# Kernel optimization log

Measured on AMD Instinct MI355X. Metric: run time of the kernel, lower is better.

Reference implementation:

```python
import jax, jax.numpy as jnp
import numpy as np
import math

B, L, H, U = 4, 4096, 1024, 1024


def setup_inputs() -> dict:
    key = jax.random.key(0)
    k_in, k_wi, k_bi, k_wo, k_bo, k_u = jax.random.split(key, 6)
    inputs = jax.random.normal(k_in, (B, L, H), dtype=jnp.float32)
    # Linear layers (torch Linear: y = x @ W.T + b), scaled like torch default init
    Wi = jax.random.normal(k_wi, (U, H), dtype=jnp.float32) / math.sqrt(H)
    bi = jax.random.normal(k_bi, (U,), dtype=jnp.float32) * 0.01
    Wo = jax.random.normal(k_wo, (H, U), dtype=jnp.float32) / math.sqrt(U)
    bo = jax.random.normal(k_bo, (H,), dtype=jnp.float32) * 0.01
    # LRU-style init of nu_log / gamma_log, exactly as in the torch __init__
    r_min, r_max = 0.9, 0.999
    u = jax.random.uniform(k_u, (U,), dtype=jnp.float32)
    nu_log = jnp.log(-0.5 * jnp.log(u * (r_max ** 2 - r_min ** 2) + r_min ** 2))
    gamma_log = jnp.log(jnp.sqrt(1.0 - jnp.exp(-jnp.exp(nu_log)) ** 2))
    params_log = jnp.stack([nu_log, gamma_log])  # [2, U]
    return {"inputs": inputs, "Wi": Wi, "bi": bi, "Wo": Wo, "bo": bo,
            "params_log": params_log}


def reference(inputs, Wi, bi, Wo, bo, params_log):
    # u = i_dense(inputs): [B, L, U]
    u = jnp.einsum('blh,uh->blu', inputs, Wi) + bi
    params = jnp.exp(params_log)
    nu, gamma = params[0], params[1]  # each [U]

    log2_L = int(np.ceil(np.log2(L)))
    pad_len = 2 ** log2_L - L
    x = jnp.pad(u, ((0, 0), (0, pad_len), (0, 0))) if pad_len else u
    Lp = 2 ** log2_L

    # Log-depth doubling parallel scan: h_t = exp(-nu) * h_{t-1} + u_t
    for i in range(1, log2_L + 1):
        l = 2 ** i
        x = x.reshape(B * Lp // l, l, U)
        x1, x2 = x[:, : l // 2], x[:, l // 2:]
        pos = jnp.arange(1, l // 2 + 1, dtype=jnp.float32)  # [l/2]
        lambs = jnp.exp(-pos[:, None] * nu)                  # [l/2, U]
        x2 = x2 + lambs * x1[:, -1:]
        x = jnp.concatenate([x1, x2], axis=1).reshape(B, Lp, U)

    x = x[:, :L] * gamma
    # o_dense: [B, L, H]
    return jnp.einsum('blu,hu->blh', x, Wo) + bo
```

## Files before the change

kernel.cpp:

```cpp
#include <hip/hip_runtime.h>

#define B_DIM 4
#define L_DIM 4096
#define H_DIM 1024
#define U_DIM 1024
#define M_DIM (B_DIM * L_DIM)
#define LC 64
#define NCH (L_DIM / LC)

using f32x4  = __attribute__((ext_vector_type(4))) float;
using bf16x8 = __attribute__((ext_vector_type(8))) __bf16;
using us8    = __attribute__((ext_vector_type(8))) unsigned short;

__device__ inline unsigned short f32_to_bf16(float f) {
  unsigned int u = __float_as_uint(f);
  u += 0x7FFF + ((u >> 16) & 1);
  return (unsigned short)(u >> 16);
}
__device__ inline float bf16_to_f32(unsigned short v) {
  return __uint_as_float((unsigned int)v << 16);
}

__device__ inline void async_load16(const void* g, void* l) {
  __builtin_amdgcn_global_load_lds(
      (const __attribute__((address_space(1))) void*)g,
      (__attribute__((address_space(3))) void*)l, 16, 0, 0);
}

#define IN_ELEMS  (M_DIM * H_DIM)
#define WI_ELEMS  (U_DIM * H_DIM)
#define WO_ELEMS  (H_DIM * U_DIM)
#define CVT_TOTAL (IN_ELEMS + WI_ELEMS + WO_ELEMS)

__global__ __launch_bounds__(256) void cvt_all(
    const float* __restrict__ inp, const float* __restrict__ wi,
    const float* __restrict__ wo,
    unsigned short* __restrict__ inp_b, unsigned short* __restrict__ wi_b,
    unsigned short* __restrict__ wo_b)
{
  size_t e = ((size_t)blockIdx.x * 256 + threadIdx.x) * 8;
  if (e >= CVT_TOTAL) return;
  const float* src; unsigned short* dst; size_t off;
  if (e < IN_ELEMS)                 { src = inp; dst = inp_b; off = e; }
  else if (e < IN_ELEMS + WI_ELEMS) { src = wi;  dst = wi_b;  off = e - IN_ELEMS; }
  else                              { src = wo;  dst = wo_b;  off = e - IN_ELEMS - WI_ELEMS; }
  f32x4 a = *(const f32x4*)(src + off);
  f32x4 b = *(const f32x4*)(src + off + 4);
  us8 r;
  r[0] = f32_to_bf16(a.x); r[1] = f32_to_bf16(a.y);
  r[2] = f32_to_bf16(a.z); r[3] = f32_to_bf16(a.w);
  r[4] = f32_to_bf16(b.x); r[5] = f32_to_bf16(b.y);
  r[6] = f32_to_bf16(b.z); r[7] = f32_to_bf16(b.w);
  *(us8*)(dst + off) = r;
}

#define TM 128
#define TN 128
#define BK 32

template <typename OUT, bool CARRY, int K>
__global__ __launch_bounds__(256) void gemm_bt_bias(
    const unsigned short* __restrict__ A, const unsigned short* __restrict__ Bm,
    const float* __restrict__ bias, OUT* __restrict__ C,
    int M, int N,
    float* __restrict__ carry_out, const float* __restrict__ params_log)
{
  __shared__ __attribute__((aligned(16))) unsigned short sA[2][TM * BK];
  __shared__ __attribute__((aligned(16))) unsigned short sB[2][TN * BK];

  const int tid    = threadIdx.x;
  const int lane   = tid & 63;
  const int wave   = tid >> 6;
  const int wm     = wave & 1;
  const int wn     = wave >> 1;
  const int frag_m = lane & 15;
  const int quad   = lane >> 4;
  const int frag_kb = 16 * (quad ^ ((lane >> 1) & 3));

  const int p    = blockIdx.y * gridDim.x + blockIdx.x;
  const int xcd  = p & 7;
  const int j    = p >> 3;
  const int slab = gridDim.y >> 3;
  const int by   = xcd * slab + (j % slab);
  const int bx   = j / slab;

  const int m0 = by * TM;
  const int n0 = bx * TN;

  const char* Ab = (const char*)A;
  const char* Bb = (const char*)Bm;
  const size_t rowbytes = (size_t)K * 2;

  const int r0s  = tid >> 2;
  const int r1s  = r0s + 64;
  const int csw  = 16 * ((tid & 3) ^ ((tid >> 3) & 3));
  const int o0   = tid * 16;
  const int o1   = o0 + 4096;

  f32x4 acc[4][4];
  #pragma unroll
  for (int i = 0; i < 4; ++i)
    #pragma unroll
    for (int jj = 0; jj < 4; ++jj)
      acc[i][jj] = {0.f, 0.f, 0.f, 0.f};

  auto stage = [&](int s, int kk) {
    const size_t kb = (size_t)kk * 2;
    async_load16(Ab + (size_t)(m0 + r0s) * rowbytes + kb + csw, (char*)sA[s] + o0);
    async_load16(Ab + (size_t)(m0 + r1s) * rowbytes + kb + csw, (char*)sA[s] + o1);
    async_load16(Bb + (size_t)(n0 + r0s) * rowbytes + kb + csw, (char*)sB[s] + o0);
    async_load16(Bb + (size_t)(n0 + r1s) * rowbytes + kb + csw, (char*)sB[s] + o1);
  };

  constexpr int NI = K / BK;
  stage(0, 0);

  #pragma unroll 2
  for (int i = 0; i < NI; ++i) {
    if (i + 1 < NI) {
      stage((i + 1) & 1, (i + 1) * BK);
      asm volatile("s_waitcnt vmcnt(4)\n\ts_barrier" ::: "memory");
    } else {
      asm volatile("s_waitcnt vmcnt(0)\n\ts_barrier" ::: "memory");
    }

    const int s = i & 1;
    bf16x8 af[4], bf[4];
    #pragma unroll
    for (int mi = 0; mi < 4; ++mi)
      af[mi] = *(const bf16x8*)((const char*)sA[s] + (wm * 64 + mi * 16 + frag_m) * 64 + frag_kb);
    #pragma unroll
    for (int ni = 0; ni < 4; ++ni)
      bf[ni] = *(const bf16x8*)((const char*)sB[s] + (wn * 64 + ni * 16 + frag_m) * 64 + frag_kb);

    #pragma unroll
    for (int mi = 0; mi < 4; ++mi)
      #pragma unroll
      for (int ni = 0; ni < 4; ++ni)
        acc[mi][ni] = __builtin_amdgcn_mfma_f32_16x16x32_bf16(af[mi], bf[ni], acc[mi][ni], 0, 0, 0);

    asm volatile("s_barrier" ::: "memory");
  }

  const int rr0 = quad * 4;
  #pragma unroll
  for (int ni = 0; ni < 4; ++ni) {
    int col  = n0 + wn * 64 + ni * 16 + frag_m;
    float bv = bias[col];
    #pragma unroll
    for (int mi = 0; mi < 4; ++mi) {
      int rowb = m0 + wm * 64 + mi * 16 + rr0;
      #pragma unroll
      for (int r = 0; r < 4; ++r) {
        float v = acc[mi][ni][r] + bv;
        if constexpr (sizeof(OUT) == 2)
          C[(size_t)(rowb + r) * N + col] = (OUT)f32_to_bf16(v);
        else
          C[(size_t)(rowb + r) * N + col] = (OUT)v;
      }
    }
  }

  if constexpr (CARRY) {
    const int chunk = (m0 >> 6) + wm;
    #pragma unroll
    for (int ni = 0; ni < 4; ++ni) {
      int col  = n0 + wn * 64 + ni * 16 + frag_m;
      float bv = bias[col];
      float nu = expf(params_log[col]);
      float w_base = expf(-nu * (float)(63 - quad * 4));
      float linv   = expf(nu);
      float l16inv = expf(16.f * nu);
      float part = 0.f;
      float wmi  = w_base;
      #pragma unroll
      for (int mi = 0; mi < 4; ++mi) {
        float w = wmi;
        #pragma unroll
        for (int r = 0; r < 4; ++r) {
          part = fmaf(w, acc[mi][ni][r] + bv, part);
          w *= linv;
        }
        wmi *= l16inv;
      }
      part += __shfl_xor(part, 16);
      part += __shfl_xor(part, 32);
      if (quad == 0)
        carry_out[(size_t)chunk * U_DIM + col] = part;
    }
  }
}

__global__ __launch_bounds__(256) void scan_prefix(
    const float* __restrict__ carry, const float* __restrict__ params_log,
    float* __restrict__ prefix)
{
  int t  = blockIdx.x * 256 + threadIdx.x;
  int b  = t >> 10;
  int uu = t & (U_DIM - 1);
  float lp = expf(-expf(params_log[uu]) * (float)LC);
  const float* cp = carry  + (size_t)b * NCH * U_DIM + uu;
  float*       pp = prefix + (size_t)b * NCH * U_DIM + uu;
  float vals[NCH];
  #pragma unroll
  for (int c = 0; c < NCH; ++c)
    vals[c] = cp[(size_t)c * U_DIM];
  float s = 0.f;
  #pragma unroll
  for (int c = 0; c < NCH; ++c) {
    pp[(size_t)c * U_DIM] = s;
    s = fmaf(s, lp, vals[c]);
  }
}

__global__ __launch_bounds__(256) void scan_apply(
    const unsigned short* __restrict__ u, const float* __restrict__ params_log,
    const float* __restrict__ prefix, unsigned short* __restrict__ x_b)
{
  int uu = blockIdx.x * 256 + threadIdx.x;
  int c  = blockIdx.y;
  int b  = blockIdx.z;
  float l = expf(-expf(params_log[uu]));
  float g = expf(params_log[U_DIM + uu]);
  float s = prefix[((size_t)b * NCH + c) * U_DIM + uu];
  const unsigned short* p = u + (size_t)(b * L_DIM + c * LC) * U_DIM + uu;
  unsigned short* q = x_b + (size_t)(b * L_DIM + c * LC) * U_DIM + uu;
  #pragma unroll 8
  for (int j = 0; j < LC; ++j) {
    s = fmaf(s, l, bf16_to_f32(p[(size_t)j * U_DIM]));
    q[(size_t)j * U_DIM] = f32_to_bf16(s * g);
  }
}

extern "C" void kernel_launch(void* const* d_in, const int* in_sizes, int n_in,
                              void* d_out, int out_size, void* d_ws, size_t ws_size,
                              hipStream_t stream)
{
  const float* inputs     = (const float*)d_in[0];
  const float* Wi         = (const float*)d_in[1];
  const float* bi         = (const float*)d_in[2];
  const float* Wo         = (const float*)d_in[3];
  const float* bo         = (const float*)d_in[4];
  const float* params_log = (const float*)d_in[5];
  float* out = (float*)d_out;

  char* ws = (char*)d_ws;
  unsigned short* u_b    = (unsigned short*)(ws);
  unsigned short* x_b    = (unsigned short*)(ws + (32u << 20));
  unsigned short* in_b   = (unsigned short*)(ws + (64u << 20));
  unsigned short* wi_b   = (unsigned short*)(ws + (96u << 20));
  unsigned short* wo_b   = (unsigned short*)(ws + (98u << 20));
  float*          carry  = (float*)(ws + (100u << 20));
  float*          prefix = (float*)(ws + (101u << 20));

  cvt_all<<<dim3((CVT_TOTAL / 8 + 255) / 256), 256, 0, stream>>>(
      inputs, Wi, Wo, in_b, wi_b, wo_b);

  gemm_bt_bias<unsigned short, true, H_DIM>
      <<<dim3(U_DIM / TN, M_DIM / TM), 256, 0, stream>>>(
      in_b, wi_b, bi, u_b, M_DIM, U_DIM, carry, params_log);

  scan_prefix<<<dim3(B_DIM * U_DIM / 256),     256, 0, stream>>>(carry, params_log, prefix);
  scan_apply <<<dim3(U_DIM / 256, NCH, B_DIM), 256, 0, stream>>>(u_b, params_log, prefix, x_b);

  gemm_bt_bias<float, false, U_DIM>
      <<<dim3(H_DIM / TN, M_DIM / TM), 256, 0, stream>>>(
      x_b, wo_b, bo, out, M_DIM, H_DIM, nullptr, nullptr);
}
```

Measured before the change: 253.6 us.

## Replace async global-to-LDS loads with register-staged prefetch in GEMM

The GEMM main loop no longer uses global_load_lds direct-to-LDS copies. It now prefetches the next K-tile into registers, runs the MFMAs on the current LDS buffer, then writes the registers into the other LDS buffer and synchronizes. The goal is to overlap global loads with compute through register staging and to drop the explicit vmcnt waits. The cost is more VGPRs and extra LDS write instructions, which could lower occupancy.

```diff
diff --git a/kernel.cpp b/kernel.cpp
--- a/kernel.cpp
+++ b/kernel.cpp
@@ -19,12 +19,6 @@
 }
 __device__ inline float bf16_to_f32(unsigned short v) {
   return __uint_as_float((unsigned int)v << 16);
-}
-
-__device__ inline void async_load16(const void* g, void* l) {
-  __builtin_amdgcn_global_load_lds(
-      (const __attribute__((address_space(1))) void*)g,
-      (__attribute__((address_space(3))) void*)l, 16, 0, 0);
 }
 
 #define IN_ELEMS  (M_DIM * H_DIM)
@@ -91,11 +85,11 @@
   const char* Bb = (const char*)Bm;
   const size_t rowbytes = (size_t)K * 2;
 
-  const int r0s  = tid >> 2;
-  const int r1s  = r0s + 64;
-  const int csw  = 16 * ((tid & 3) ^ ((tid >> 3) & 3));
-  const int o0   = tid * 16;
-  const int o1   = o0 + 4096;
+  const int r0s = tid >> 2;
+  const int r1s = r0s + 64;
+  const int cg  = tid & 3;
+  const int lo0 = r0s * 64 + 16 * (cg ^ ((tid >> 3) & 3));
+  const int lo1 = lo0 + 4096;
 
   f32x4 acc[4][4];
   #pragma unroll
@@ -104,25 +98,29 @@
     for (int jj = 0; jj < 4; ++jj)
       acc[i][jj] = {0.f, 0.f, 0.f, 0.f};
 
-  auto stage = [&](int s, int kk) {
-    const size_t kb = (size_t)kk * 2;
-    async_load16(Ab + (size_t)(m0 + r0s) * rowbytes + kb + csw, (char*)sA[s] + o0);
-    async_load16(Ab + (size_t)(m0 + r1s) * rowbytes + kb + csw, (char*)sA[s] + o1);
-    async_load16(Bb + (size_t)(n0 + r0s) * rowbytes + kb + csw, (char*)sB[s] + o0);
-    async_load16(Bb + (size_t)(n0 + r1s) * rowbytes + kb + csw, (char*)sB[s] + o1);
+  us8 pa0, pa1, pb0, pb1;
+  auto gload = [&](int kk) {
+    const size_t kb = (size_t)kk * 2 + cg * 16;
+    pa0 = *(const us8*)(Ab + (size_t)(m0 + r0s) * rowbytes + kb);
+    pa1 = *(const us8*)(Ab + (size_t)(m0 + r1s) * rowbytes + kb);
+    pb0 = *(const us8*)(Bb + (size_t)(n0 + r0s) * rowbytes + kb);
+    pb1 = *(const us8*)(Bb + (size_t)(n0 + r1s) * rowbytes + kb);
   };
+  auto swrite = [&](int s) {
+    *(us8*)((char*)sA[s] + lo0) = pa0;
+    *(us8*)((char*)sA[s] + lo1) = pa1;
+    *(us8*)((char*)sB[s] + lo0) = pb0;
+    *(us8*)((char*)sB[s] + lo1) = pb1;
+  };
 
   constexpr int NI = K / BK;
-  stage(0, 0);
-
-  #pragma unroll 2
+  gload(0);
+  swrite(0);
+  __syncthreads();
+
   for (int i = 0; i < NI; ++i) {
-    if (i + 1 < NI) {
-      stage((i + 1) & 1, (i + 1) * BK);
-      asm volatile("s_waitcnt vmcnt(4)\n\ts_barrier" ::: "memory");
-    } else {
-      asm volatile("s_waitcnt vmcnt(0)\n\ts_barrier" ::: "memory");
-    }
+    if (i + 1 < NI)
+      gload((i + 1) * BK);
 
     const int s = i & 1;
     bf16x8 af[4], bf[4];
@@ -139,7 +137,10 @@
       for (int ni = 0; ni < 4; ++ni)
         acc[mi][ni] = __builtin_amdgcn_mfma_f32_16x16x32_bf16(af[mi], bf[ni], acc[mi][ni], 0, 0, 0);
 
-    asm volatile("s_barrier" ::: "memory");
+    if (i + 1 < NI) {
+      swrite((i + 1) & 1);
+      __syncthreads();
+    }
   }
 
   const int rr0 = quad * 4;
```

Measured after the change: 253.2 us. Within noise of the previous version (-0.2%).
